# Kernel tuning notes

Measured on AMD Instinct MI355X. Metric: run time of the kernel, lower is better.

## Reference

```python
import jax, jax.numpy as jnp
import numpy as np

EPS = 1e-5

def conv3x3(x, w):
    # x: [B,C,H,W], w: [O,I,3,3]
    return jax.lax.conv_general_dilated(x, w, (1, 1), 'SAME',
                                        dimension_numbers=('NCHW', 'OIHW', 'NCHW'))

def bn_relu(x, g, b):
    # training-mode batchnorm: batch stats over (B,H,W)
    mean = jnp.mean(x, axis=(0, 2, 3), keepdims=True)
    var = jnp.var(x, axis=(0, 2, 3), keepdims=True)
    xn = (x - mean) * jax.lax.rsqrt(var + EPS)
    return jax.nn.relu(xn * g[None, :, None, None] + b[None, :, None, None])

def self_attention(x, qw, qb, kw, kb, vw, vb, gamma):
    # x: [B,C,H,W]; qw/kw: [C//8,C]; vw: [C,C]
    B, C, H, W = x.shape
    xf = x.reshape(B, C, H * W)                       # [B,C,N]
    q = jnp.einsum('dc,bcn->bdn', qw, xf) + qb[None, :, None]
    k = jnp.einsum('dc,bcn->bdn', kw, xf) + kb[None, :, None]
    v = jnp.einsum('dc,bcn->bdn', vw, xf) + vb[None, :, None]
    energy = jnp.einsum('bdi,bdj->bij', q, k)         # [B,N,N]
    attn = jax.nn.softmax(energy, axis=-1)
    out = jnp.einsum('bcj,bij->bci', v, attn)         # [B,C,N]
    return (gamma * out + xf).reshape(B, C, H, W)

def setup_inputs() -> dict:
    key = jax.random.key(0)
    ks = jax.random.split(key, 16)
    C = 64
    s = 0.05
    inp = {
        'x': jax.random.normal(ks[0], (4, 3, 64, 64), jnp.float32),
        'c1_w': jax.random.normal(ks[1], (C, 3, 3, 3), jnp.float32) * s,
        'bn1_g': jnp.ones((C,), jnp.float32),
        'bn1_b': jnp.zeros((C,), jnp.float32),
        'c2_w': jax.random.normal(ks[2], (C, C, 3, 3), jnp.float32) * s,
        'bn2_g': jnp.ones((C,), jnp.float32),
        'bn2_b': jnp.zeros((C,), jnp.float32),
        # 4 attention blocks, stacked along leading axis
        'qw': jax.random.normal(ks[3], (4, C // 8, C), jnp.float32) * s,
        'qb': jnp.zeros((4, C // 8), jnp.float32),
        'kw': jax.random.normal(ks[4], (4, C // 8, C), jnp.float32) * s,
        'kb': jnp.zeros((4, C // 8), jnp.float32),
        'vw': jax.random.normal(ks[5], (4, C, C), jnp.float32) * s,
        'vb': jnp.zeros((4, C), jnp.float32),
        'gammas': jnp.full((4,), 0.1, jnp.float32),   # torch inits to 0; 0.1 to exercise the path
        'out_w': jax.random.normal(ks[6], (1, C), jnp.float32) * s,
        'out_b': jnp.zeros((1,), jnp.float32),
    }
    return inp

def reference(x, c1_w, bn1_g, bn1_b, c2_w, bn2_g, bn2_b,
              qw, qb, kw, kb, vw, vb, gammas, out_w, out_b):
    h = bn_relu(conv3x3(x, c1_w), bn1_g, bn1_b)
    h = bn_relu(conv3x3(h, c2_w), bn2_g, bn2_b)
    for i in range(4):
        h = self_attention(h, qw[i], qb[i], kw[i], kb[i], vw[i], vb[i], gammas[i])
    B, C, H, W = h.shape
    out = jnp.einsum('oc,bchw->bohw', out_w, h) + out_b[None, :, None, None]
    return out
```

## Files before the change

### kernel.cpp

```cpp
#include <hip/hip_runtime.h>

#define BN_EPS 1e-5f
#define LOG2E 1.44269504f

typedef __attribute__((ext_vector_type(8))) short short8v;
typedef __attribute__((ext_vector_type(4))) float float4v;
typedef __attribute__((ext_vector_type(4))) unsigned uint4v;

__device__ inline unsigned short f2bf(float f) {
    unsigned u = __float_as_uint(f);
    u += 0x7fffu + ((u >> 16) & 1u);
    return (unsigned short)(u >> 16);
}

__device__ inline float fexp2(float x) { return __builtin_amdgcn_exp2f(x); }

__device__ inline unsigned cvtpk_bf16(float lo, float hi) {
    unsigned r;
    asm("v_cvt_pk_bf16_f32 %0, %1, %2" : "=v"(r) : "v"(lo), "v"(hi));
    return r;
}

#define GLOAD_LDS(gp, lp) __builtin_amdgcn_global_load_lds( \
    (const __attribute__((address_space(1))) void*)(gp),    \
    (__attribute__((address_space(3))) void*)(lp), 16, 0, 0)

__global__ void conv1_kernel(const float* __restrict__ x, const float* __restrict__ w,
                             float* __restrict__ out) {
    int idx = blockIdx.x * 256 + threadIdx.x;
    int xx = idx & 63, y = (idx >> 6) & 63, o = (idx >> 12) & 63, b = idx >> 18;
    float acc = 0.f;
    #pragma unroll
    for (int i = 0; i < 3; ++i) {
        #pragma unroll
        for (int dy = 0; dy < 3; ++dy) {
            int gy = y + dy - 1;
            if (gy < 0 || gy > 63) continue;
            #pragma unroll
            for (int dx = 0; dx < 3; ++dx) {
                int gx = xx + dx - 1;
                if (gx < 0 || gx > 63) continue;
                acc += w[o*27 + i*9 + dy*3 + dx] * x[(b*3 + i)*4096 + gy*64 + gx];
            }
        }
    }
    out[idx] = acc;
}

__global__ void stats_part_kernel(const float* __restrict__ t, float* __restrict__ ps) {
    int bc = blockIdx.x;
    int tid = threadIdx.x;
    const float4* p4 = (const float4*)(t + (size_t)bc * 4096);
    float s = 0.f, s2 = 0.f;
    for (int n = tid; n < 1024; n += 256) {
        float4 v = p4[n];
        s  += (v.x + v.y) + (v.z + v.w);
        s2 += (v.x*v.x + v.y*v.y) + (v.z*v.z + v.w*v.w);
    }
    #pragma unroll
    for (int off = 32; off > 0; off >>= 1) {
        s  += __shfl_down(s, off);
        s2 += __shfl_down(s2, off);
    }
    __shared__ float ls[8];
    int wv = tid >> 6, ln = tid & 63;
    if (ln == 0) { ls[wv] = s; ls[4+wv] = s2; }
    __syncthreads();
    if (tid == 0) {
        ps[bc]       = ls[0]+ls[1]+ls[2]+ls[3];
        ps[256 + bc] = ls[4]+ls[5]+ls[6]+ls[7];
    }
}

__global__ void stats_final_kernel(const float* __restrict__ ps, float* __restrict__ stats) {
    int c = threadIdx.x;
    float S = 0.f, S2 = 0.f;
    #pragma unroll
    for (int b = 0; b < 4; ++b) { S += ps[b*64 + c]; S2 += ps[256 + b*64 + c]; }
    float mean = S / 16384.f;
    float var = S2 / 16384.f - mean*mean;
    stats[c] = mean;
    stats[64+c] = rsqrtf(fmaxf(var, 0.f) + BN_EPS);
}

__global__ void bnrelu_kernel(float* __restrict__ t, const float* __restrict__ stats,
                              const float* __restrict__ g, const float* __restrict__ bb) {
    int idx = blockIdx.x * 256 + threadIdx.x;
    int e0 = idx << 2;
    int c = (e0 >> 12) & 63;
    float mean = stats[c], rstd = stats[64+c], gg = g[c], bbv = bb[c];
    float4 v = ((const float4*)t)[idx];
    v.x = (v.x - mean) * rstd * gg + bbv; v.x = v.x > 0.f ? v.x : 0.f;
    v.y = (v.y - mean) * rstd * gg + bbv; v.y = v.y > 0.f ? v.y : 0.f;
    v.z = (v.z - mean) * rstd * gg + bbv; v.z = v.z > 0.f ? v.z : 0.f;
    v.w = (v.w - mean) * rstd * gg + bbv; v.w = v.w > 0.f ? v.w : 0.f;
    ((float4*)t)[idx] = v;
}

__global__ __launch_bounds__(256) void bnrelu_t_kernel(const float* __restrict__ t,
        const float* __restrict__ stats, const float* __restrict__ g,
        const float* __restrict__ bb, unsigned short* __restrict__ xT) {
    int b = blockIdx.y, n0 = blockIdx.x * 64;
    int tid = threadIdx.x;
    int ln = tid & 63, r0 = tid >> 6;
    __shared__ float xs[64][65];
    for (int c = r0; c < 64; c += 4) {
        float mean = stats[c], rstd = stats[64+c] * g[c], bbv = bb[c];
        float v = t[(size_t)(b*64 + c)*4096 + n0 + ln];
        v = (v - mean) * rstd + bbv;
        xs[c][ln] = v > 0.f ? v : 0.f;
    }
    __syncthreads();
    int n_l = tid >> 2, cg = tid & 3;
    int c0 = cg * 16;
    uint4v pk0, pk1;
    #pragma unroll
    for (int e = 0; e < 4; ++e) {
        pk0[e] = cvtpk_bf16(xs[c0 + 2*e][n_l],     xs[c0 + 2*e + 1][n_l]);
        pk1[e] = cvtpk_bf16(xs[c0 + 8 + 2*e][n_l], xs[c0 + 8 + 2*e + 1][n_l]);
    }
    unsigned short* op = xT + ((size_t)b*4096 + n0 + n_l) * 64 + c0;
    *(uint4v*)op = pk0;
    *(uint4v*)(op + 8) = pk1;
}

__global__ void wprep_kernel(const float* __restrict__ w, unsigned short* __restrict__ wT) {
    int idx = blockIdx.x * 256 + threadIdx.x;
    int ci = idx & 63, o = (idx >> 6) & 63, t = idx >> 12;
    wT[idx] = f2bf(w[o*576 + ci*9 + t]);
}

__global__ __launch_bounds__(512) void conv2_mfma_kernel(
        const unsigned short* __restrict__ xT, const unsigned short* __restrict__ wT,
        float* __restrict__ out) {
    int b = blockIdx.y;
    int y = blockIdx.x;
    int tid = threadIdx.x;
    int w8 = tid >> 6, ln = tid & 63;
    int ot = w8 & 3, nh = w8 >> 2;
    int li = ln & 15, g = ln >> 4;
    int obase = ot * 16;

    const unsigned short* xb = xT + (size_t)b * 4096 * 64;
    const short8v zf = {0,0,0,0,0,0,0,0};

    short8v af0[9], af1[9];
    #pragma unroll
    for (int t = 0; t < 9; ++t) {
        const unsigned short* wrow = wT + ((size_t)t*64 + obase + li) * 64 + 8*g;
        af0[t] = *(const short8v*)(wrow);
        af1[t] = *(const short8v*)(wrow + 32);
    }

    float4v acc0 = {0.f,0.f,0.f,0.f}, acc1 = {0.f,0.f,0.f,0.f};
    int nA = y*64 + nh*32 + li;
    int nB = nA + 16;
    int xA = nA & 63, xB = nB & 63;

    #pragma unroll
    for (int t = 0; t < 9; ++t) {
        int dy = t/3 - 1, dx = (t%3) - 1;
        bool rowok = (y + dy >= 0) && (y + dy <= 63);
        int sh = dy*64 + dx;
        bool okA = rowok && (xA + dx >= 0) && (xA + dx <= 63);
        bool okB = rowok && (xB + dx >= 0) && (xB + dx <= 63);
        const unsigned short* xrA = xb + (size_t)(okA ? nA + sh : nA) * 64 + 8*g;
        const unsigned short* xrB = xb + (size_t)(okB ? nB + sh : nB) * 64 + 8*g;
        short8v bA0 = *(const short8v*)(xrA);
        short8v bA1 = *(const short8v*)(xrA + 32);
        short8v bB0 = *(const short8v*)(xrB);
        short8v bB1 = *(const short8v*)(xrB + 32);
        if (!okA) { bA0 = zf; bA1 = zf; }
        if (!okB) { bB0 = zf; bB1 = zf; }
        acc0 = __builtin_amdgcn_mfma_f32_16x16x32_bf16(af0[t], bA0, acc0, 0, 0, 0);
        acc0 = __builtin_amdgcn_mfma_f32_16x16x32_bf16(af1[t], bA1, acc0, 0, 0, 0);
        acc1 = __builtin_amdgcn_mfma_f32_16x16x32_bf16(af0[t], bB0, acc1, 0, 0, 0);
        acc1 = __builtin_amdgcn_mfma_f32_16x16x32_bf16(af1[t], bB1, acc1, 0, 0, 0);
    }

    #pragma unroll
    for (int r = 0; r < 4; ++r) {
        int o = obase + 4*g + r;
        size_t base = ((size_t)(b*64 + o)) * 4096;
        out[base + nA] = acc0[r];
        out[base + nB] = acc1[r];
    }
}

__global__ __launch_bounds__(512) void qkv_kernel(const float* __restrict__ h,
    const float* __restrict__ qw, const float* __restrict__ qb,
    const float* __restrict__ kw, const float* __restrict__ kb,
    const float* __restrict__ vw, const float* __restrict__ vb,
    int a,
    unsigned short* __restrict__ qT, unsigned short* __restrict__ kT,
    unsigned short* __restrict__ vB) {
    int b = blockIdx.y;
    int n0 = blockIdx.x * 64;
    int tid = threadIdx.x;
    int nl = tid & 63, r0 = tid >> 6;
    __shared__ float xsh[64][64];
    __shared__ float wsh[80][64];
    __shared__ float bsh[80];
    for (int e = tid; e < 4096; e += 512) {
        int c = e >> 6, n = e & 63;
        xsh[c][n] = h[(size_t)(b*64 + c)*4096 + n0 + n];
    }
    for (int e = tid; e < 5120; e += 512) {
        int r = e >> 6, c = e & 63;
        float wv;
        if (r < 8)       wv = qw[a*512 + r*64 + c];
        else if (r < 16) wv = kw[a*512 + (r-8)*64 + c];
        else             wv = vw[a*4096 + (r-16)*64 + c];
        wsh[r][c] = wv;
    }
    if (tid < 80) {
        float bv;
        if (tid < 8)       bv = qb[a*8 + tid];
        else if (tid < 16) bv = kb[a*8 + tid - 8];
        else               bv = vb[a*64 + tid - 16];
        bsh[tid] = bv;
    }
    __syncthreads();
    int n = n0 + nl;
    for (int r = r0; r < 80; r += 8) {
        float acc = bsh[r];
        #pragma unroll 8
        for (int c = 0; c < 64; ++c) acc += wsh[r][c] * xsh[c][nl];
        if (r < 8) {
            qT[((size_t)b*4096 + n)*8 + r] = f2bf(acc * LOG2E);
        } else if (r < 16) {
            kT[((size_t)b*4096 + n)*8 + (r-8)] = f2bf(acc);
        } else {
            vB[((size_t)b*64 + (r-16))*4096 + n] = f2bf(acc);
        }
    }
}

__global__ __launch_bounds__(256) void flash_split_kernel(
    const unsigned short* __restrict__ qT, const unsigned short* __restrict__ kT,
    const unsigned short* __restrict__ vB,
    float* __restrict__ accO0, float* __restrict__ accP,
    float* __restrict__ lP) {
    int b = blockIdx.z;
    int js = blockIdx.y;
    int tid = threadIdx.x;
    int w = tid >> 6, ln = tid & 63;
    int li = ln & 15, g = ln >> 4;
    int i0 = blockIdx.x * 64 + w * 16;

    const unsigned short* qTb = qT + (size_t)b * 4096 * 8;
    const unsigned short* kTb = kT + (size_t)b * 4096 * 8;
    const unsigned short* vBb = vB + (size_t)b * 64 * 4096;

    __shared__ unsigned short kbuf[2][512];
    __shared__ unsigned short vbuf[2][4096];

    const short8v zf = {0,0,0,0,0,0,0,0};
    short8v qf = zf;
    if (g == 0) qf = *(const short8v*)(qTb + (size_t)(i0 + li) * 8);

    int jp = 2*li - (li & 3);
    int kA0 = jp*8, kA1 = (jp+4)*8, kB0 = (jp+32)*8, kB1 = (jp+36)*8;
    int vroff = li*64;
    int ch0 = ((g    ) ^ (li & 7)) * 8;
    int ch1 = ((4 + g) ^ (li & 7)) * 8;
    size_t vq0 = (size_t)(w*8 + (ln >> 3)) * 4096 + 8*((ln & 7) ^ (ln >> 3));
    size_t vq1 = vq0 + (size_t)32 * 4096;

    float lsum = 0.f;
    float4v acc0 = {0.f,0.f,0.f,0.f}, acc1 = {0.f,0.f,0.f,0.f};
    float4v acc2 = {0.f,0.f,0.f,0.f}, acc3 = {0.f,0.f,0.f,0.f};

    int jbase = js * 1024;

    if (w == 0) GLOAD_LDS(kTb + (size_t)(jbase + ln) * 8, &kbuf[0][0]);
    GLOAD_LDS(vBb + vq0 + jbase, &vbuf[0][w * 512]);
    GLOAD_LDS(vBb + vq1 + jbase, &vbuf[0][(w + 4) * 512]);

    for (int t = 0; t < 16; ++t) {
        int cur = t & 1;
        if (t < 15) {
            int j0n = jbase + (t + 1) * 64;
            if (w == 0) GLOAD_LDS(kTb + (size_t)(j0n + ln) * 8, &kbuf[cur ^ 1][0]);
            GLOAD_LDS(vBb + vq0 + j0n, &vbuf[cur ^ 1][w * 512]);
            GLOAD_LDS(vBb + vq1 + j0n, &vbuf[cur ^ 1][(w + 4) * 512]);
            if (w == 0) asm volatile("s_waitcnt vmcnt(3)" ::: "memory");
            else        asm volatile("s_waitcnt vmcnt(2)" ::: "memory");
        } else {
            asm volatile("s_waitcnt vmcnt(0)" ::: "memory");
        }
        __builtin_amdgcn_s_barrier();

        const unsigned short* kb = &kbuf[cur][0];
        const unsigned short* vb = &vbuf[cur][0];

        short8v kfA0 = *(const short8v*)(kb + kA0);
        short8v kfA1 = *(const short8v*)(kb + kA1);
        short8v kfB0 = *(const short8v*)(kb + kB0);
        short8v kfB1 = *(const short8v*)(kb + kB1);
        float4v sA0 = {0.f,0.f,0.f,0.f}, sA1 = {0.f,0.f,0.f,0.f};
        float4v sB0 = {0.f,0.f,0.f,0.f}, sB1 = {0.f,0.f,0.f,0.f};
        sA0 = __builtin_amdgcn_mfma_f32_16x16x32_bf16(kfA0, qf, sA0, 0, 0, 0);
        sA1 = __builtin_amdgcn_mfma_f32_16x16x32_bf16(kfA1, qf, sA1, 0, 0, 0);
        sB0 = __builtin_amdgcn_mfma_f32_16x16x32_bf16(kfB0, qf, sB0, 0, 0, 0);
        sB1 = __builtin_amdgcn_mfma_f32_16x16x32_bf16(kfB1, qf, sB1, 0, 0, 0);

        float pA0 = fexp2(sA0[0]), pA1 = fexp2(sA0[1]);
        float pA2 = fexp2(sA0[2]), pA3 = fexp2(sA0[3]);
        float pA4 = fexp2(sA1[0]), pA5 = fexp2(sA1[1]);
        float pA6 = fexp2(sA1[2]), pA7 = fexp2(sA1[3]);
        float pB0 = fexp2(sB0[0]), pB1 = fexp2(sB0[1]);
        float pB2 = fexp2(sB0[2]), pB3 = fexp2(sB0[3]);
        float pB4 = fexp2(sB1[0]), pB5 = fexp2(sB1[1]);
        float pB6 = fexp2(sB1[2]), pB7 = fexp2(sB1[3]);
        lsum += (((pA0 + pA1) + (pA2 + pA3)) + ((pA4 + pA5) + (pA6 + pA7)))
              + (((pB0 + pB1) + (pB2 + pB3)) + ((pB4 + pB5) + (pB6 + pB7)));
        uint4v piA, piB;
        piA[0] = cvtpk_bf16(pA0, pA1); piA[1] = cvtpk_bf16(pA2, pA3);
        piA[2] = cvtpk_bf16(pA4, pA5); piA[3] = cvtpk_bf16(pA6, pA7);
        piB[0] = cvtpk_bf16(pB0, pB1); piB[1] = cvtpk_bf16(pB2, pB3);
        piB[2] = cvtpk_bf16(pB4, pB5); piB[3] = cvtpk_bf16(pB6, pB7);
        short8v pfA = __builtin_bit_cast(short8v, piA);
        short8v pfB = __builtin_bit_cast(short8v, piB);

        {
            short8v va = *(const short8v*)(vb + vroff + ch0);
            short8v v2 = *(const short8v*)(vb + vroff + ch1);
            acc0 = __builtin_amdgcn_mfma_f32_16x16x32_bf16(va, pfA, acc0, 0, 0, 0);
            acc0 = __builtin_amdgcn_mfma_f32_16x16x32_bf16(v2, pfB, acc0, 0, 0, 0);
        }
        {
            short8v va = *(const short8v*)(vb + 1024 + vroff + ch0);
            short8v v2 = *(const short8v*)(vb + 1024 + vroff + ch1);
            acc1 = __builtin_amdgcn_mfma_f32_16x16x32_bf16(va, pfA, acc1, 0, 0, 0);
            acc1 = __builtin_amdgcn_mfma_f32_16x16x32_bf16(v2, pfB, acc1, 0, 0, 0);
        }
        {
            short8v va = *(const short8v*)(vb + 2048 + vroff + ch0);
            short8v v2 = *(const short8v*)(vb + 2048 + vroff + ch1);
            acc2 = __builtin_amdgcn_mfma_f32_16x16x32_bf16(va, pfA, acc2, 0, 0, 0);
            acc2 = __builtin_amdgcn_mfma_f32_16x16x32_bf16(v2, pfB, acc2, 0, 0, 0);
        }
        {
            short8v va = *(const short8v*)(vb + 3072 + vroff + ch0);
            short8v v2 = *(const short8v*)(vb + 3072 + vroff + ch1);
            acc3 = __builtin_amdgcn_mfma_f32_16x16x32_bf16(va, pfA, acc3, 0, 0, 0);
            acc3 = __builtin_amdgcn_mfma_f32_16x16x32_bf16(v2, pfB, acc3, 0, 0, 0);
        }
        __builtin_amdgcn_s_barrier();
    }
    lsum += __shfl_xor(lsum, 16);
    lsum += __shfl_xor(lsum, 32);

    float* accO = (js == 0) ? accO0 : (accP + (size_t)(js - 1) * 1048576);
    int i = i0 + li;
    #pragma unroll
    for (int r = 0; r < 4; ++r) {
        int c = 4*g + r;
        accO[((size_t)(b*64 + c      )) * 4096 + i] = acc0[r];
        accO[((size_t)(b*64 + c + 16)) * 4096 + i] = acc1[r];
        accO[((size_t)(b*64 + c + 32)) * 4096 + i] = acc2[r];
        accO[((size_t)(b*64 + c + 48)) * 4096 + i] = acc3[r];
    }
    if (g == 0) {
        lP[(size_t)(b*4 + js)*4096 + i] = lsum;
    }
}

__global__ void merge_kernel(float* __restrict__ acc0io, const float* __restrict__ accP,
                             const float* __restrict__ lP,
                             const float* __restrict__ hin,
                             const float* __restrict__ gammas, int a) {
    int idx = blockIdx.x * 256 + threadIdx.x;
    int e0 = idx << 2;
    int b = e0 >> 18, i0 = e0 & 4095;
    float gamma = gammas[a];
    float4 l0 = *(const float4*)&lP[(size_t)(b*4 + 0)*4096 + i0];
    float4 l1 = *(const float4*)&lP[(size_t)(b*4 + 1)*4096 + i0];
    float4 l2 = *(const float4*)&lP[(size_t)(b*4 + 2)*4096 + i0];
    float4 l3 = *(const float4*)&lP[(size_t)(b*4 + 3)*4096 + i0];
    float4 a0 = ((const float4*)acc0io)[idx];
    float4 a1 = ((const float4*)accP)[idx];
    float4 a2 = ((const float4*)accP)[idx + 262144];
    float4 a3 = ((const float4*)accP)[idx + 524288];
    float4 hv = ((const float4*)hin)[idx];
    float4 o;
    #pragma unroll
    for (int t = 0; t < 4; ++t) {
        float l = ((const float*)&l0)[t] + ((const float*)&l1)[t]
                + ((const float*)&l2)[t] + ((const float*)&l3)[t];
        float num = ((const float*)&a0)[t] + ((const float*)&a1)[t]
                  + ((const float*)&a2)[t] + ((const float*)&a3)[t];
        ((float*)&o)[t] = num * (gamma / l) + ((const float*)&hv)[t];
    }
    ((float4*)acc0io)[idx] = o;
}

__global__ void proj_kernel(const float* __restrict__ h, const float* __restrict__ ow,
                            const float* __restrict__ ob, float* __restrict__ out) {
    int blk = blockIdx.x;
    int b = blk >> 6, ch = blk & 63;
    int tid = threadIdx.x;
    int hw = ch*64 + (tid & 63), cs = tid >> 6;
    float acc = 0.f;
    #pragma unroll 4
    for (int c = cs; c < 64; c += 4) acc += ow[c] * h[(size_t)(b*64 + c)*4096 + hw];
    __shared__ float red[4][64];
    red[cs][tid & 63] = acc;
    __syncthreads();
    if (tid < 64) {
        float s = red[0][tid] + red[1][tid] + red[2][tid] + red[3][tid] + ob[0];
        out[(size_t)b*4096 + ch*64 + tid] = s;
    }
}

extern "C" void kernel_launch(void* const* d_in, const int* in_sizes, int n_in,
                              void* d_out, int out_size, void* d_ws, size_t ws_size,
                              hipStream_t stream) {
    const float* x    = (const float*)d_in[0];
    const float* c1w  = (const float*)d_in[1];
    const float* bn1g = (const float*)d_in[2];
    const float* bn1b = (const float*)d_in[3];
    const float* c2w  = (const float*)d_in[4];
    const float* bn2g = (const float*)d_in[5];
    const float* bn2b = (const float*)d_in[6];
    const float* qw   = (const float*)d_in[7];
    const float* qbb  = (const float*)d_in[8];
    const float* kw   = (const float*)d_in[9];
    const float* kbb  = (const float*)d_in[10];
    const float* vw   = (const float*)d_in[11];
    const float* vbb  = (const float*)d_in[12];
    const float* gam  = (const float*)d_in[13];
    const float* ow   = (const float*)d_in[14];
    const float* ob   = (const float*)d_in[15];
    float* out = (float*)d_out;

    float* t1 = (float*)d_ws;
    float* t2 = t1 + 1048576;
    unsigned short* qT = (unsigned short*)(t2 + 1048576);
    unsigned short* kT = qT + 131072;
    unsigned short* vB = kT + 131072;
    float* accP  = (float*)(vB + 1048576);
    float* lP    = accP + 3*1048576;
    float* stats = lP + 65536;
    float* ps    = stats + 128;
    unsigned short* wT = (unsigned short*)(ps + 512);
    unsigned short* xT = (unsigned short*)accP;

    wprep_kernel<<<144, 256, 0, stream>>>(c2w, wT);
    conv1_kernel<<<4096, 256, 0, stream>>>(x, c1w, t1);
    stats_part_kernel<<<256, 256, 0, stream>>>(t1, ps);
    stats_final_kernel<<<1, 64, 0, stream>>>(ps, stats);
    bnrelu_t_kernel<<<dim3(64,4), 256, 0, stream>>>(t1, stats, bn1g, bn1b, xT);
    conv2_mfma_kernel<<<dim3(64,4), 512, 0, stream>>>(xT, wT, t2);
    stats_part_kernel<<<256, 256, 0, stream>>>(t2, ps);
    stats_final_kernel<<<1, 64, 0, stream>>>(ps, stats);
    bnrelu_kernel<<<1024, 256, 0, stream>>>(t2, stats, bn2g, bn2b);

    float* cur = t2; float* oth = t1;
    for (int a = 0; a < 4; ++a) {
        qkv_kernel<<<dim3(64,4), 512, 0, stream>>>(cur, qw, qbb, kw, kbb, vw, vbb, a, qT, kT, vB);
        flash_split_kernel<<<dim3(64,4,4), 256, 0, stream>>>(qT, kT, vB, oth, accP, lP);
        merge_kernel<<<1024, 256, 0, stream>>>(oth, accP, lP, cur, gam, a);
        float* tmp = cur; cur = oth; oth = tmp;
    }
    proj_kernel<<<256, 256, 0, stream>>>(cur, ow, ob, out);
}
```

Measured before the change: 288.3 us.

## Use MFMA for QKV projection and fuse second BN-ReLU into consumers

Rewrites the QKV projection as a bf16 MFMA kernel that loads its weight fragments straight into registers, replacing the scalar LDS dot-product loop. The standalone BN2+ReLU pass is removed. Normalization is instead applied on the fly inside the first attention block's QKV and merge kernels, behind a flag. This saves one full read-write pass over the activation and cuts FMA work. The cost is that the BN math runs twice, and every block reloads and converts the weights from global memory.

Measured after the change: 267.5 us. 7.2% less time.

```diff
diff --git a/kernel.cpp b/kernel.cpp
--- a/kernel.cpp
+++ b/kernel.cpp
@@ -6,6 +6,7 @@
 typedef __attribute__((ext_vector_type(8))) short short8v;
 typedef __attribute__((ext_vector_type(4))) float float4v;
 typedef __attribute__((ext_vector_type(4))) unsigned uint4v;
+typedef __attribute__((ext_vector_type(2))) unsigned uint2v;
 
 __device__ inline unsigned short f2bf(float f) {
     unsigned u = __float_as_uint(f);
@@ -81,20 +82,6 @@
     float var = S2 / 16384.f - mean*mean;
     stats[c] = mean;
     stats[64+c] = rsqrtf(fmaxf(var, 0.f) + BN_EPS);
-}
-
-__global__ void bnrelu_kernel(float* __restrict__ t, const float* __restrict__ stats,
-                              const float* __restrict__ g, const float* __restrict__ bb) {
-    int idx = blockIdx.x * 256 + threadIdx.x;
-    int e0 = idx << 2;
-    int c = (e0 >> 12) & 63;
-    float mean = stats[c], rstd = stats[64+c], gg = g[c], bbv = bb[c];
-    float4 v = ((const float4*)t)[idx];
-    v.x = (v.x - mean) * rstd * gg + bbv; v.x = v.x > 0.f ? v.x : 0.f;
-    v.y = (v.y - mean) * rstd * gg + bbv; v.y = v.y > 0.f ? v.y : 0.f;
-    v.z = (v.z - mean) * rstd * gg + bbv; v.z = v.z > 0.f ? v.z : 0.f;
-    v.w = (v.w - mean) * rstd * gg + bbv; v.w = v.w > 0.f ? v.w : 0.f;
-    ((float4*)t)[idx] = v;
 }
 
 __global__ __launch_bounds__(256) void bnrelu_t_kernel(const float* __restrict__ t,
@@ -187,52 +174,113 @@
     }
 }
 
-__global__ __launch_bounds__(512) void qkv_kernel(const float* __restrict__ h,
+__global__ __launch_bounds__(256) void qkv_mfma_kernel(const float* __restrict__ h,
     const float* __restrict__ qw, const float* __restrict__ qb,
     const float* __restrict__ kw, const float* __restrict__ kb,
     const float* __restrict__ vw, const float* __restrict__ vb,
-    int a,
+    const float* __restrict__ stats, const float* __restrict__ g2,
+    const float* __restrict__ b2, int a, int bnflag,
     unsigned short* __restrict__ qT, unsigned short* __restrict__ kT,
     unsigned short* __restrict__ vB) {
     int b = blockIdx.y;
-    int n0 = blockIdx.x * 64;
     int tid = threadIdx.x;
-    int nl = tid & 63, r0 = tid >> 6;
-    __shared__ float xsh[64][64];
-    __shared__ float wsh[80][64];
-    __shared__ float bsh[80];
-    for (int e = tid; e < 4096; e += 512) {
-        int c = e >> 6, n = e & 63;
-        xsh[c][n] = h[(size_t)(b*64 + c)*4096 + n0 + n];
-    }
-    for (int e = tid; e < 5120; e += 512) {
-        int r = e >> 6, c = e & 63;
-        float wv;
-        if (r < 8)       wv = qw[a*512 + r*64 + c];
-        else if (r < 16) wv = kw[a*512 + (r-8)*64 + c];
-        else             wv = vw[a*4096 + (r-16)*64 + c];
-        wsh[r][c] = wv;
-    }
-    if (tid < 80) {
-        float bv;
-        if (tid < 8)       bv = qb[a*8 + tid];
-        else if (tid < 16) bv = kb[a*8 + tid - 8];
-        else               bv = vb[a*64 + tid - 16];
-        bsh[tid] = bv;
-    }
-    __syncthreads();
-    int n = n0 + nl;
-    for (int r = r0; r < 80; r += 8) {
-        float acc = bsh[r];
-        #pragma unroll 8
-        for (int c = 0; c < 64; ++c) acc += wsh[r][c] * xsh[c][nl];
-        if (r < 8) {
-            qT[((size_t)b*4096 + n)*8 + r] = f2bf(acc * LOG2E);
-        } else if (r < 16) {
-            kT[((size_t)b*4096 + n)*8 + (r-8)] = f2bf(acc);
-        } else {
-            vB[((size_t)b*64 + (r-16))*4096 + n] = f2bf(acc);
-        }
+    int w = tid >> 6, ln = tid & 63;
+    int li = ln & 15, g = ln >> 4;
+    int n = blockIdx.x * 64 + w * 16 + li;
+
+    const float* hb = h + (size_t)b * 64 * 4096 + n;
+
+    short8v wf[5][2];
+    {
+        const float* src0;
+        float scale = 1.f;
+        if (li < 8) { src0 = qw + a*512 + li*64; scale = LOG2E; }
+        else        { src0 = kw + a*512 + (li-8)*64; }
+        #pragma unroll
+        for (int kh = 0; kh < 2; ++kh) {
+            uint4v pk;
+            #pragma unroll
+            for (int e = 0; e < 4; ++e)
+                pk[e] = cvtpk_bf16(src0[kh*32 + 8*g + 2*e] * scale,
+                                   src0[kh*32 + 8*g + 2*e + 1] * scale);
+            wf[0][kh] = __builtin_bit_cast(short8v, pk);
+        }
+        #pragma unroll
+        for (int rt = 1; rt < 5; ++rt) {
+            const float* src = vw + a*4096 + (rt*16 - 16 + li)*64;
+            #pragma unroll
+            for (int kh = 0; kh < 2; ++kh) {
+                uint4v pk;
+                #pragma unroll
+                for (int e = 0; e < 4; ++e)
+                    pk[e] = cvtpk_bf16(src[kh*32 + 8*g + 2*e],
+                                       src[kh*32 + 8*g + 2*e + 1]);
+                wf[rt][kh] = __builtin_bit_cast(short8v, pk);
+            }
+        }
+    }
+
+    float4v acc0, acc1, acc2, acc3, acc4;
+    {
+        int r4 = 4*g;
+        #pragma unroll
+        for (int r = 0; r < 4; ++r) {
+            int row = r4 + r;
+            acc0[r] = (row < 8) ? qb[a*8 + row] * LOG2E : kb[a*8 + row - 8];
+            acc1[r] = vb[a*64 + 0  + row];
+            acc2[r] = vb[a*64 + 16 + row];
+            acc3[r] = vb[a*64 + 32 + row];
+            acc4[r] = vb[a*64 + 48 + row];
+        }
+    }
+
+    short8v hf0, hf1;
+    #pragma unroll
+    for (int kh = 0; kh < 2; ++kh) {
+        uint4v pk;
+        #pragma unroll
+        for (int e = 0; e < 4; ++e) {
+            int c0 = kh*32 + 8*g + 2*e;
+            float x0 = hb[(size_t)c0 * 4096];
+            float x1 = hb[(size_t)(c0 + 1) * 4096];
+            if (bnflag) {
+                float rv0 = stats[64+c0] * g2[c0], rv1 = stats[64+c0+1] * g2[c0+1];
+                x0 = (x0 - stats[c0]) * rv0 + b2[c0];
+                x1 = (x1 - stats[c0+1]) * rv1 + b2[c0+1];
+                x0 = x0 > 0.f ? x0 : 0.f;
+                x1 = x1 > 0.f ? x1 : 0.f;
+            }
+            pk[e] = cvtpk_bf16(x0, x1);
+        }
+        if (kh == 0) hf0 = __builtin_bit_cast(short8v, pk);
+        else         hf1 = __builtin_bit_cast(short8v, pk);
+    }
+
+    acc0 = __builtin_amdgcn_mfma_f32_16x16x32_bf16(wf[0][0], hf0, acc0, 0, 0, 0);
+    acc0 = __builtin_amdgcn_mfma_f32_16x16x32_bf16(wf[0][1], hf1, acc0, 0, 0, 0);
+    acc1 = __builtin_amdgcn_mfma_f32_16x16x32_bf16(wf[1][0], hf0, acc1, 0, 0, 0);
+    acc1 = __builtin_amdgcn_mfma_f32_16x16x32_bf16(wf[1][1], hf1, acc1, 0, 0, 0);
+    acc2 = __builtin_amdgcn_mfma_f32_16x16x32_bf16(wf[2][0], hf0, acc2, 0, 0, 0);
+    acc2 = __builtin_amdgcn_mfma_f32_16x16x32_bf16(wf[2][1], hf1, acc2, 0, 0, 0);
+    acc3 = __builtin_amdgcn_mfma_f32_16x16x32_bf16(wf[3][0], hf0, acc3, 0, 0, 0);
+    acc3 = __builtin_amdgcn_mfma_f32_16x16x32_bf16(wf[3][1], hf1, acc3, 0, 0, 0);
+    acc4 = __builtin_amdgcn_mfma_f32_16x16x32_bf16(wf[4][0], hf0, acc4, 0, 0, 0);
+    acc4 = __builtin_amdgcn_mfma_f32_16x16x32_bf16(wf[4][1], hf1, acc4, 0, 0, 0);
+
+    {
+        uint2v pk;
+        pk[0] = cvtpk_bf16(acc0[0], acc0[1]);
+        pk[1] = cvtpk_bf16(acc0[2], acc0[3]);
+        if (g < 2) *(uint2v*)(qT + ((size_t)b*4096 + n)*8 + 4*g) = pk;
+        else       *(uint2v*)(kT + ((size_t)b*4096 + n)*8 + 4*g - 8) = pk;
+    }
+    #pragma unroll
+    for (int r = 0; r < 4; ++r) {
+        int row = 4*g + r;
+        vB[((size_t)(b*64 + 0  + row))*4096 + n] = f2bf(acc1[r]);
+        vB[((size_t)(b*64 + 16 + row))*4096 + n] = f2bf(acc2[r]);
+        vB[((size_t)(b*64 + 32 + row))*4096 + n] = f2bf(acc3[r]);
+        vB[((size_t)(b*64 + 48 + row))*4096 + n] = f2bf(acc4[r]);
     }
 }
 
@@ -370,10 +418,13 @@
 __global__ void merge_kernel(float* __restrict__ acc0io, const float* __restrict__ accP,
                              const float* __restrict__ lP,
                              const float* __restrict__ hin,
+                             const float* __restrict__ stats, const float* __restrict__ g2,
+                             const float* __restrict__ b2, int bnflag,
                              const float* __restrict__ gammas, int a) {
     int idx = blockIdx.x * 256 + threadIdx.x;
     int e0 = idx << 2;
     int b = e0 >> 18, i0 = e0 & 4095;
+    int c = (e0 >> 12) & 63;
     float gamma = gammas[a];
     float4 l0 = *(const float4*)&lP[(size_t)(b*4 + 0)*4096 + i0];
     float4 l1 = *(const float4*)&lP[(size_t)(b*4 + 1)*4096 + i0];
@@ -384,6 +435,13 @@
     float4 a2 = ((const float4*)accP)[idx + 262144];
     float4 a3 = ((const float4*)accP)[idx + 524288];
     float4 hv = ((const float4*)hin)[idx];
+    if (bnflag) {
+        float mean = stats[c], rv = stats[64+c] * g2[c], bv = b2[c];
+        hv.x = (hv.x - mean) * rv + bv; hv.x = hv.x > 0.f ? hv.x : 0.f;
+        hv.y = (hv.y - mean) * rv + bv; hv.y = hv.y > 0.f ? hv.y : 0.f;
+        hv.z = (hv.z - mean) * rv + bv; hv.z = hv.z > 0.f ? hv.z : 0.f;
+        hv.w = (hv.w - mean) * rv + bv; hv.w = hv.w > 0.f ? hv.w : 0.f;
+    }
     float4 o;
     #pragma unroll
     for (int t = 0; t < 4; ++t) {
@@ -455,13 +513,16 @@
     conv2_mfma_kernel<<<dim3(64,4), 512, 0, stream>>>(xT, wT, t2);
     stats_part_kernel<<<256, 256, 0, stream>>>(t2, ps);
     stats_final_kernel<<<1, 64, 0, stream>>>(ps, stats);
-    bnrelu_kernel<<<1024, 256, 0, stream>>>(t2, stats, bn2g, bn2b);
 
     float* cur = t2; float* oth = t1;
     for (int a = 0; a < 4; ++a) {
-        qkv_kernel<<<dim3(64,4), 512, 0, stream>>>(cur, qw, qbb, kw, kbb, vw, vbb, a, qT, kT, vB);
+        int bnflag = (a == 0) ? 1 : 0;
+        qkv_mfma_kernel<<<dim3(64,4), 256, 0, stream>>>(cur, qw, qbb, kw, kbb, vw, vbb,
+                                                        stats, bn2g, bn2b, a, bnflag,
+                                                        qT, kT, vB);
         flash_split_kernel<<<dim3(64,4,4), 256, 0, stream>>>(qT, kT, vB, oth, accP, lP);
-        merge_kernel<<<1024, 256, 0, stream>>>(oth, accP, lP, cur, gam, a);
+        merge_kernel<<<1024, 256, 0, stream>>>(oth, accP, lP, cur,
+                                               stats, bn2g, bn2b, bnflag, gam, a);
         float* tmp = cur; cur = oth; oth = tmp;
     }
     proj_kernel<<<256, 256, 0, stream>>>(cur, ow, ob, out);
```
